# Optimization experiments

Hardware: AMD Instinct MI355X
Metric: run time of the kernel (lower is better)

Reference implementation:

```python
import itertools
import jax, jax.numpy as jnp
import numpy as np

B, S, D = 512, 49, 448
H, KD, RATIO, RES = 8, 32, 4, 7
EKD = KD * RATIO              # expanded key dim = 128
QKV_OUT = H * (2 * KD + EKD)  # 1536
MLP_HID = D * 4               # 1792
EPS = 1e-5
LS_INIT = 1e-5


def _build_bias_idxs():
    points = list(itertools.product(range(RES), range(RES)))
    offsets = {}
    idxs = []
    for p1 in points:
        for p2 in points:
            off = (abs(p1[0] - p2[0]), abs(p1[1] - p2[1]))
            if off not in offsets:
                offsets[off] = len(offsets)
            idxs.append(offsets[off])
    return np.asarray(idxs, dtype=np.int32).reshape(len(points), len(points)), len(offsets)


def setup_inputs() -> dict:
    key = jax.random.key(0)
    ks = jax.random.split(key, 10)
    idxs_np, n_off = _build_bias_idxs()  # (49,49), 49 unique offsets
    std = 0.02
    return {
        "hidden_states": jax.random.normal(ks[0], (B, S, D), jnp.float32),
        "ln1_g": jnp.ones((D,), jnp.float32),
        "ln1_b": jnp.zeros((D,), jnp.float32),
        "qkv_w": jax.random.normal(ks[1], (D, QKV_OUT), jnp.float32) * std,
        "qkv_b": jnp.zeros((QKV_OUT,), jnp.float32),
        "attention_biases": jax.random.normal(ks[2], (H, n_off), jnp.float32) * std,
        "proj_w": jax.random.normal(ks[3], (H * EKD, D), jnp.float32) * std,
        "proj_b": jnp.zeros((D,), jnp.float32),
        "ln2_g": jnp.ones((D,), jnp.float32),
        "ln2_b": jnp.zeros((D,), jnp.float32),
        "mlp_w1": jax.random.normal(ks[4], (D, MLP_HID), jnp.float32) * std,
        "mlp_b1": jnp.zeros((MLP_HID,), jnp.float32),
        "mlp_w2": jax.random.normal(ks[5], (MLP_HID, D), jnp.float32) * std,
        "mlp_b2": jnp.zeros((D,), jnp.float32),
        "ls1": jnp.full((D,), LS_INIT, jnp.float32),
        "ls2": jnp.full((D,), LS_INIT, jnp.float32),
        "attention_bias_idxs": jnp.asarray(idxs_np),
    }


def _layernorm(x, g, b):
    mu = jnp.mean(x, axis=-1, keepdims=True)
    var = jnp.mean(jnp.square(x - mu), axis=-1, keepdims=True)
    return (x - mu) * jax.lax.rsqrt(var + EPS) * g + b


def reference(hidden_states, ln1_g, ln1_b, qkv_w, qkv_b, attention_biases,
              proj_w, proj_b, ln2_g, ln2_b, mlp_w1, mlp_b1, mlp_w2, mlp_b2,
              ls1, ls2, attention_bias_idxs):
    x = hidden_states
    # --- token mixer (self-attention with relative-position bias) ---
    h = _layernorm(x, ln1_g, ln1_b)
    qkv = h @ qkv_w + qkv_b                           # [B,S,1536]
    qkv = qkv.reshape(B, S, H, 2 * KD + EKD)
    q, k, v = jnp.split(qkv, [KD, 2 * KD], axis=3)    # [B,S,H,32/32/128]
    scale = KD ** (-0.5)
    scores = jnp.einsum("bqhd,bkhd->bhqk", q, k) * scale
    bias = attention_biases[:, attention_bias_idxs]   # [H,S,S]
    probs = jax.nn.softmax(scores + bias[None], axis=-1)
    ctx = jnp.einsum("bhqk,bkhd->bqhd", probs, v).reshape(B, S, H * EKD)
    attn_out = ctx @ proj_w + proj_b                  # [B,S,D]
    # --- residual with layerscale (drop_path = identity in eval) ---
    x = x + ls1 * attn_out
    # --- MLP branch ---
    h2 = _layernorm(x, ln2_g, ln2_b)
    m = jax.nn.gelu(h2 @ mlp_w1 + mlp_b1, approximate=False)
    m = m @ mlp_w2 + mlp_b2
    x = x + ls2 * m
    return x
```

## Files before the change

kernel.cpp:

```cpp
#include <hip/hip_runtime.h>
#include <hip/hip_bf16.h>

#define BB 512
#define SS 49
#define DD 448
#define HH 8
#define QKVO 1536
#define MLPH 1792
#define MM (BB*SS)

using bf16_t = __hip_bfloat16;
typedef __attribute__((ext_vector_type(8))) short short8;
typedef __attribute__((ext_vector_type(4))) float f32x4;

__device__ __forceinline__ void gload_lds16(const void* g, void* l) {
  __builtin_amdgcn_global_load_lds(
      (const __attribute__((address_space(1))) void*)g,
      (__attribute__((address_space(3))) void*)l,
      16, 0, 0);
}

__global__ void prep_kernel(const float* __restrict__ qkv_w, const float* __restrict__ proj_w,
                            const float* __restrict__ w1, const float* __restrict__ w2,
                            const float* __restrict__ ab, const int* __restrict__ idxs,
                            bf16_t* __restrict__ qkv_wT, bf16_t* __restrict__ proj_wT,
                            bf16_t* __restrict__ w1T, bf16_t* __restrict__ w2T,
                            bf16_t* __restrict__ bias_pad)
{
  int idx = blockIdx.x * 256 + threadIdx.x;
  if (idx < 688128) {
    int n = idx / 448, k = idx % 448;
    qkv_wT[idx] = __float2bfloat16(qkv_w[k*1536 + n]);
  } else if ((idx -= 688128) < 458752) {
    int n = idx / 1024, k = idx % 1024;
    proj_wT[idx] = __float2bfloat16(proj_w[k*448 + n]);
  } else if ((idx -= 458752) < 802816) {
    int n = idx / 448, k = idx % 448;
    w1T[idx] = __float2bfloat16(w1[k*1792 + n]);
  } else if ((idx -= 802816) < 802816) {
    int n = idx / 1792, k = idx % 1792;
    w2T[idx] = __float2bfloat16(w2[k*448 + n]);
  } else if ((idx -= 802816) < 32768) {
    int h = idx >> 12, r = (idx >> 6) & 63, c = idx & 63;
    float v = (r < SS && c < SS) ? ab[h*49 + idxs[r*49 + c]] : -1e30f;
    bias_pad[idx] = __float2bfloat16(v);
  }
}

__global__ __launch_bounds__(256) void ln_kernel(const float* __restrict__ x,
                                                 const float* __restrict__ g,
                                                 const float* __restrict__ b,
                                                 bf16_t* __restrict__ out)
{
  const int w = threadIdx.x >> 6, lane = threadIdx.x & 63;
  const int row = blockIdx.x * 4 + w;
  const float* xr = x + (size_t)row * DD;
  float v[7];
  float s = 0.f;
#pragma unroll
  for (int j = 0; j < 7; ++j) { v[j] = xr[lane + 64*j]; s += v[j]; }
#pragma unroll
  for (int off = 32; off; off >>= 1) s += __shfl_xor(s, off, 64);
  const float mu = s * (1.0f/448.0f);
  float q = 0.f;
#pragma unroll
  for (int j = 0; j < 7; ++j) { float d = v[j] - mu; q += d*d; }
#pragma unroll
  for (int off = 32; off; off >>= 1) q += __shfl_xor(q, off, 64);
  const float rstd = rsqrtf(q * (1.0f/448.0f) + 1e-5f);
  bf16_t* orow = out + (size_t)row * DD;
#pragma unroll
  for (int j = 0; j < 7; ++j) {
    int c = lane + 64*j;
    orow[c] = __float2bfloat16((v[j] - mu) * rstd * g[c] + b[c]);
  }
}

__global__ __launch_bounds__(256) void red1_ln2_kernel(
    const float* __restrict__ x, const bf16_t* __restrict__ p0,
    const bf16_t* __restrict__ p1, const float* __restrict__ pb,
    const float* __restrict__ ls1, const float* __restrict__ g,
    const float* __restrict__ b, float* __restrict__ out, bf16_t* __restrict__ h2)
{
  const int w = threadIdx.x >> 6, lane = threadIdx.x & 63;
  const int row = blockIdx.x * 4 + w;
  const float* xr = x + (size_t)row * DD;
  const bf16_t* p0r = p0 + (size_t)row * DD;
  const bf16_t* p1r = p1 + (size_t)row * DD;
  float* orow = out + (size_t)row * DD;
  float v[7];
  float s = 0.f;
#pragma unroll
  for (int j = 0; j < 7; ++j) {
    const int c = lane + 64*j;
    const float pv = __bfloat162float(p0r[c]) + __bfloat162float(p1r[c]) + pb[c];
    v[j] = xr[c] + ls1[c] * pv;
    orow[c] = v[j];
    s += v[j];
  }
#pragma unroll
  for (int off = 32; off; off >>= 1) s += __shfl_xor(s, off, 64);
  const float mu = s * (1.0f/448.0f);
  float q = 0.f;
#pragma unroll
  for (int j = 0; j < 7; ++j) { float d = v[j] - mu; q += d*d; }
#pragma unroll
  for (int off = 32; off; off >>= 1) q += __shfl_xor(q, off, 64);
  const float rstd = rsqrtf(q * (1.0f/448.0f) + 1e-5f);
  bf16_t* hrow = h2 + (size_t)row * DD;
#pragma unroll
  for (int j = 0; j < 7; ++j) {
    const int c = lane + 64*j;
    hrow[c] = __float2bfloat16((v[j] - mu) * rstd * g[c] + b[c]);
  }
}

__global__ __launch_bounds__(256) void red2_kernel(
    const bf16_t* __restrict__ q0, const bf16_t* __restrict__ q1,
    const float* __restrict__ pb, const float* __restrict__ ls2,
    float* __restrict__ out)
{
  const int w = threadIdx.x >> 6, lane = threadIdx.x & 63;
  const int row = blockIdx.x * 4 + w;
  const bf16_t* q0r = q0 + (size_t)row * DD;
  const bf16_t* q1r = q1 + (size_t)row * DD;
  float* orow = out + (size_t)row * DD;
#pragma unroll
  for (int j = 0; j < 7; ++j) {
    const int c = lane + 64*j;
    const float pv = __bfloat162float(q0r[c]) + __bfloat162float(q1r[c]) + pb[c];
    orow[c] = orow[c] + ls2[c] * pv;
  }
}

enum { EP_BF16 = 0, EP_GELU = 2, EP_PART = 4 };

template<int EPI, int NSPLIT>
__global__ __launch_bounds__(256, 2) void gemmr_bf16(
    const bf16_t* __restrict__ A, const bf16_t* __restrict__ Bt,
    const float* __restrict__ bias, bf16_t* __restrict__ O0,
    bf16_t* __restrict__ O1, int N, int K, int gy)
{
  __shared__ __align__(16) char lds[32768];
  const int t = threadIdx.x;
  const int lane = t & 63;
  const int w = t >> 6;

  const int chunk = gridDim.x >> 3;
  const int swz = (blockIdx.x & 7) * chunk + (blockIdx.x >> 3);
  const int m0 = (swz / (gy * NSPLIT)) * 128;
  const int rr = swz % (gy * NSPLIT);
  const int n0 = (rr / NSPLIT) * 128;
  const int sp = rr % NSPLIT;
  const int ksub = K / NSPLIT;
  const int kbase = sp * ksub;

  const int fr = lane & 15;
  const int fq = lane >> 4;
  const int wm = (w >> 1) * 64;
  const int wn = (w & 1) * 64;

  f32x4 acc[4][4];
#pragma unroll
  for (int i = 0; i < 4; ++i)
#pragma unroll
    for (int j = 0; j < 4; ++j)
      acc[i][j] = f32x4{0.f, 0.f, 0.f, 0.f};

  const int rsub = t >> 3;
  const int g8 = (t & 7) ^ (rsub & 7);
  const int wbase = w * 1024;
  const int nkt = ksub >> 6;

  const bf16_t* gA[4];
  const bf16_t* gB[4];
#pragma unroll
  for (int i = 0; i < 4; ++i) {
    gA[i] = A + (size_t)(m0 + i*32 + rsub) * K + kbase + g8*8;
    int rb = n0 + i*32 + rsub;
    if (rb >= N) rb = N - 1;
    gB[i] = Bt + (size_t)rb * K + kbase + g8*8;
  }

  for (int kt = 0; kt < nkt; ++kt) {
    const int ko = kt << 6;
#pragma unroll
    for (int i = 0; i < 4; ++i) {
      gload_lds16(gA[i] + ko, lds + i*4096 + wbase);
      gload_lds16(gB[i] + ko, lds + 16384 + i*4096 + wbase);
    }
    __syncthreads();
#pragma unroll
    for (int kk = 0; kk < 2; ++kk) {
      short8 af[4], bfr[4];
#pragma unroll
      for (int i = 0; i < 4; ++i) {
        const int ra = wm + i*16 + fr;
        const int ca = (fq + kk*4) ^ (ra & 7);
        af[i] = *(const short8*)(lds + ra*128 + ca*16);
        const int rb2 = wn + i*16 + fr;
        const int cb = (fq + kk*4) ^ (rb2 & 7);
        bfr[i] = *(const short8*)(lds + 16384 + rb2*128 + cb*16);
      }
#pragma unroll
      for (int mi = 0; mi < 4; ++mi)
#pragma unroll
        for (int ni = 0; ni < 4; ++ni)
          acc[mi][ni] = __builtin_amdgcn_mfma_f32_16x16x32_bf16(af[mi], bfr[ni], acc[mi][ni], 0, 0, 0);
    }
    __syncthreads();
  }

  bf16_t* P = (NSPLIT == 2 && sp == 1) ? O1 : O0;
#pragma unroll
  for (int mi = 0; mi < 4; ++mi) {
#pragma unroll
    for (int ni = 0; ni < 4; ++ni) {
      const int col = n0 + wn + ni*16 + fr;
      if (col < N) {
        float bc = 0.f;
        if constexpr (EPI != EP_PART) bc = bias[col];
        const int row0 = m0 + wm + mi*16 + fq*4;
#pragma unroll
        for (int ri = 0; ri < 4; ++ri) {
          const size_t o = (size_t)(row0 + ri) * N + col;
          const float v = acc[mi][ni][ri] + bc;
          if constexpr (EPI == EP_GELU) {
            P[o] = __float2bfloat16(0.5f * v * (1.0f + erff(v * 0.7071067811865475f)));
          } else {
            P[o] = __float2bfloat16(v);
          }
        }
      }
    }
  }
}

__global__ __launch_bounds__(64) void attn_mfma_kernel(const bf16_t* __restrict__ qkv,
                                                       const bf16_t* __restrict__ bias_pad,
                                                       bf16_t* __restrict__ ctx)
{
  __shared__ __align__(16) bf16_t VsF[64*128];
  __shared__ __align__(16) bf16_t PsF[64*72];
  const int b = blockIdx.x >> 3, h = blockIdx.x & 7;
  const int l = threadIdx.x;
  const int fr = l & 15, g = l >> 4;
  const size_t base = ((size_t)b * SS) * QKVO + (size_t)h * 192;

  for (int c = l; c < 1024; c += 64) {
    const int j = c >> 4, ch = c & 15;
    const int jc = j < SS ? j : SS - 1;
    short8 v = *(const short8*)(qkv + base + (size_t)jc * QKVO + 64 + ch*8);
    *(short8*)(&VsF[j*128 + ((ch ^ (j >> 3)) & 15)*8]) = v;
  }

  short8 qf[4], kf[4];
#pragma unroll
  for (int mi = 0; mi < 4; ++mi) {
    int qr = mi*16 + fr; if (qr > SS-1) qr = SS-1;
    qf[mi] = *(const short8*)(qkv + base + (size_t)qr * QKVO + g*8);
    int kr = mi*16 + fr; if (kr > SS-1) kr = SS-1;
    kf[mi] = *(const short8*)(qkv + base + (size_t)kr * QKVO + 32 + g*8);
  }
  f32x4 sc[4][4];
#pragma unroll
  for (int mi = 0; mi < 4; ++mi)
#pragma unroll
    for (int ni = 0; ni < 4; ++ni)
      sc[mi][ni] = f32x4{0.f,0.f,0.f,0.f};
#pragma unroll
  for (int mi = 0; mi < 4; ++mi)
#pragma unroll
    for (int ni = 0; ni < 4; ++ni)
      sc[mi][ni] = __builtin_amdgcn_mfma_f32_16x16x32_bf16(qf[mi], kf[ni], sc[mi][ni], 0, 0, 0);

  const float scale = 0.17677669529663687f;
  const bf16_t* bp = bias_pad + (size_t)h * 4096;
#pragma unroll
  for (int mi = 0; mi < 4; ++mi) {
#pragma unroll
    for (int ri = 0; ri < 4; ++ri) {
      const int r = mi*16 + g*4 + ri;
      float v0 = sc[mi][0][ri]*scale + __bfloat162float(bp[r*64 +      fr]);
      float v1 = sc[mi][1][ri]*scale + __bfloat162float(bp[r*64 + 16 + fr]);
      float v2 = sc[mi][2][ri]*scale + __bfloat162float(bp[r*64 + 32 + fr]);
      float v3 = sc[mi][3][ri]*scale + __bfloat162float(bp[r*64 + 48 + fr]);
      float m = fmaxf(fmaxf(v0, v1), fmaxf(v2, v3));
#pragma unroll
      for (int off = 8; off; off >>= 1) m = fmaxf(m, __shfl_xor(m, off, 64));
      v0 = __expf(v0 - m); v1 = __expf(v1 - m);
      v2 = __expf(v2 - m); v3 = __expf(v3 - m);
      float s = v0 + v1 + v2 + v3;
#pragma unroll
      for (int off = 8; off; off >>= 1) s += __shfl_xor(s, off, 64);
      const float inv = 1.0f / s;
      PsF[r*72 +      fr] = __float2bfloat16(v0 * inv);
      PsF[r*72 + 16 + fr] = __float2bfloat16(v1 * inv);
      PsF[r*72 + 32 + fr] = __float2bfloat16(v2 * inv);
      PsF[r*72 + 48 + fr] = __float2bfloat16(v3 * inv);
    }
  }
  __syncthreads();

  short8 pf[4][2];
#pragma unroll
  for (int mi = 0; mi < 4; ++mi)
#pragma unroll
    for (int ks = 0; ks < 2; ++ks)
      pf[mi][ks] = *(const short8*)(&PsF[(mi*16 + fr)*72 + ks*32 + g*8]);

#pragma unroll
  for (int ni = 0; ni < 8; ++ni) {
    const int e = ni*16 + fr;
    short8 vf[2];
#pragma unroll
    for (int ks = 0; ks < 2; ++ks) {
      const int jb = ks*32 + g*8;
#pragma unroll
      for (int jj = 0; jj < 8; ++jj) {
        const int j = jb + jj;
        const int ch = ((e >> 3) ^ (j >> 3)) & 15;
        vf[ks][jj] = *(const short*)(&VsF[j*128 + ch*8 + (e & 7)]);
      }
    }
    f32x4 acc2[4];
#pragma unroll
    for (int mi = 0; mi < 4; ++mi) acc2[mi] = f32x4{0.f,0.f,0.f,0.f};
#pragma unroll
    for (int ks = 0; ks < 2; ++ks)
#pragma unroll
      for (int mi = 0; mi < 4; ++mi)
        acc2[mi] = __builtin_amdgcn_mfma_f32_16x16x32_bf16(pf[mi][ks], vf[ks], acc2[mi], 0, 0, 0);
#pragma unroll
    for (int mi = 0; mi < 4; ++mi) {
#pragma unroll
      for (int ri = 0; ri < 4; ++ri) {
        const int q = mi*16 + g*4 + ri;
        if (q < SS)
          ctx[((size_t)b * SS + q) * 1024 + h*128 + e] = __float2bfloat16(acc2[mi][ri]);
      }
    }
  }
}

extern "C" void kernel_launch(void* const* d_in, const int* in_sizes, int n_in,
                              void* d_out, int out_size, void* d_ws, size_t ws_size,
                              hipStream_t stream) {
  const float* x      = (const float*)d_in[0];
  const float* ln1_g  = (const float*)d_in[1];
  const float* ln1_b  = (const float*)d_in[2];
  const float* qkv_w  = (const float*)d_in[3];
  const float* qkv_b  = (const float*)d_in[4];
  const float* ab     = (const float*)d_in[5];
  const float* proj_w = (const float*)d_in[6];
  const float* proj_b = (const float*)d_in[7];
  const float* ln2_g  = (const float*)d_in[8];
  const float* ln2_b  = (const float*)d_in[9];
  const float* w1     = (const float*)d_in[10];
  const float* b1     = (const float*)d_in[11];
  const float* w2     = (const float*)d_in[12];
  const float* b2     = (const float*)d_in[13];
  const float* ls1    = (const float*)d_in[14];
  const float* ls2    = (const float*)d_in[15];
  const int*   idxs   = (const int*)d_in[16];
  float* out = (float*)d_out;
  char* ws = (char*)d_ws;

  bf16_t* h_buf    = (bf16_t*)(ws);
  bf16_t* qkv_buf  = (bf16_t*)(ws + 22478848);
  bf16_t* ctx_buf  = (bf16_t*)(ws + 99549184);
  bf16_t* m_buf    = (bf16_t*)(ws + 22478848);
  bf16_t* p0       = (bf16_t*)(ws + 22478848);
  bf16_t* p1       = (bf16_t*)(ws + 44957696);
  bf16_t* q0       = (bf16_t*)(ws);
  bf16_t* q1       = (bf16_t*)(ws + 112394240);
  bf16_t* qkv_wT   = (bf16_t*)(ws + 150929408);
  bf16_t* proj_wT  = (bf16_t*)(ws + 152305664);
  bf16_t* w1T      = (bf16_t*)(ws + 153223168);
  bf16_t* w2T      = (bf16_t*)(ws + 154828800);
  bf16_t* bias_pad = (bf16_t*)(ws + 156434432);

  const int prep_total = 688128 + 458752 + 802816 + 802816 + 32768;
  prep_kernel<<<(prep_total + 255)/256, 256, 0, stream>>>(
      qkv_w, proj_w, w1, w2, ab, idxs, qkv_wT, proj_wT, w1T, w2T, bias_pad);

  ln_kernel<<<MM/4, 256, 0, stream>>>(x, ln1_g, ln1_b, h_buf);

  gemmr_bf16<EP_BF16, 1><<<196*12, 256, 0, stream>>>(
      h_buf, qkv_wT, qkv_b, qkv_buf, nullptr, QKVO, DD, 12);

  attn_mfma_kernel<<<BB*HH, 64, 0, stream>>>(qkv_buf, bias_pad, ctx_buf);

  gemmr_bf16<EP_PART, 2><<<196*4*2, 256, 0, stream>>>(
      ctx_buf, proj_wT, nullptr, p0, p1, DD, 1024, 4);

  red1_ln2_kernel<<<MM/4, 256, 0, stream>>>(
      x, p0, p1, proj_b, ls1, ln2_g, ln2_b, out, h_buf);

  gemmr_bf16<EP_GELU, 1><<<196*14, 256, 0, stream>>>(
      h_buf, w1T, b1, m_buf, nullptr, MLPH, DD, 14);

  gemmr_bf16<EP_PART, 2><<<196*4*2, 256, 0, stream>>>(
      m_buf, w2T, nullptr, q0, q1, DD, MLPH, 4);

  red2_kernel<<<MM/4, 256, 0, stream>>>(q0, q1, b2, ls2, out);
}
```

Before: 324.8 us.

## Add 256x128-tile bf16 GEMM with XCD-aware block remap for QKV and MLP1

Adds a new 512-thread bf16 MFMA GEMM with 256x128 output tiles, a K-step of 64 staged through swizzled LDS via direct global-to-LDS loads, and a block remap that gives each XCD a contiguous range of tiles. The bias and GELU epilogue is written through LDS so rows are stored with wide 16-byte writes. It replaces the 128x128 kernel for the QKV projection and the first MLP GEMM, aiming for more operand reuse per tile and better L2 locality. The LDS tile is single-buffered and uses about 68 KB, which limits occupancy below the declared launch bound. Load latency may therefore not be hidden well across the seven K iterations.

```diff
diff --git a/kernel.cpp b/kernel.cpp
--- a/kernel.cpp
+++ b/kernel.cpp
@@ -134,6 +134,116 @@
 }
 
 enum { EP_BF16 = 0, EP_GELU = 2, EP_PART = 4 };
+
+template<int EPI>
+__global__ __launch_bounds__(512, 4) void gemm256_bf16(
+    const bf16_t* __restrict__ A, const bf16_t* __restrict__ Bt,
+    const float* __restrict__ bias, bf16_t* __restrict__ O,
+    int N, int K, int gy)
+{
+  __shared__ __align__(16) char lds[69632];
+  const int t = threadIdx.x;
+  const int lane = t & 63;
+  const int w = t >> 6;
+
+  const int nwg = gridDim.x;
+  const int q8 = nwg >> 3, r8 = nwg & 7;
+  const int xcd = blockIdx.x & 7, bix = blockIdx.x >> 3;
+  const int wg = (xcd < r8 ? xcd*(q8+1) : r8*(q8+1) + (xcd-r8)*q8) + bix;
+  const int m0 = (wg / gy) * 256;
+  const int n0 = (wg % gy) * 128;
+
+  const int fr = lane & 15;
+  const int fq = lane >> 4;
+  const int wm = (w >> 1) * 64;
+  const int wn = (w & 1) * 64;
+
+  f32x4 acc[4][4];
+#pragma unroll
+  for (int i = 0; i < 4; ++i)
+#pragma unroll
+    for (int j = 0; j < 4; ++j)
+      acc[i][j] = f32x4{0.f, 0.f, 0.f, 0.f};
+
+  const int rsub = t >> 3;
+  const int g8 = (t & 7) ^ (rsub & 7);
+  const int wbase = w * 1024;
+  const int nkt = K >> 6;
+
+  const bf16_t* gA[4];
+  const bf16_t* gB[2];
+#pragma unroll
+  for (int i = 0; i < 4; ++i)
+    gA[i] = A + (size_t)(m0 + i*64 + rsub) * K + g8*8;
+#pragma unroll
+  for (int i = 0; i < 2; ++i) {
+    int rb = n0 + i*64 + rsub;
+    if (rb >= N) rb = N - 1;
+    gB[i] = Bt + (size_t)rb * K + g8*8;
+  }
+
+  for (int kt = 0; kt < nkt; ++kt) {
+    const int ko = kt << 6;
+#pragma unroll
+    for (int i = 0; i < 4; ++i)
+      gload_lds16(gA[i] + ko, lds + i*8192 + wbase);
+#pragma unroll
+    for (int i = 0; i < 2; ++i)
+      gload_lds16(gB[i] + ko, lds + 32768 + i*8192 + wbase);
+    __syncthreads();
+#pragma unroll
+    for (int kk = 0; kk < 2; ++kk) {
+      short8 af[4], bfr[4];
+#pragma unroll
+      for (int i = 0; i < 4; ++i) {
+        const int ra = wm + i*16 + fr;
+        const int ca = (fq + kk*4) ^ (ra & 7);
+        af[i] = *(const short8*)(lds + ra*128 + ca*16);
+        const int rb2 = wn + i*16 + fr;
+        const int cb = (fq + kk*4) ^ (rb2 & 7);
+        bfr[i] = *(const short8*)(lds + 32768 + rb2*128 + cb*16);
+      }
+#pragma unroll
+      for (int mi = 0; mi < 4; ++mi)
+#pragma unroll
+        for (int ni = 0; ni < 4; ++ni)
+          acc[mi][ni] = __builtin_amdgcn_mfma_f32_16x16x32_bf16(af[mi], bfr[ni], acc[mi][ni], 0, 0, 0);
+    }
+    __syncthreads();
+  }
+
+  bf16_t* lbf = (bf16_t*)lds;
+#pragma unroll
+  for (int mi = 0; mi < 4; ++mi) {
+#pragma unroll
+    for (int ni = 0; ni < 4; ++ni) {
+      const int col = wn + ni*16 + fr;
+      const float bc = bias[n0 + col];
+      const int row0 = wm + mi*16 + fq*4;
+#pragma unroll
+      for (int ri = 0; ri < 4; ++ri) {
+        float v = acc[mi][ni][ri] + bc;
+        if constexpr (EPI == EP_GELU)
+          v = 0.5f * v * (1.0f + erff(v * 0.7071067811865475f));
+        lbf[(row0 + ri)*136 + col] = __float2bfloat16(v);
+      }
+    }
+  }
+  __syncthreads();
+
+  const int rl = t >> 3;
+  const int ll = t & 7;
+#pragma unroll
+  for (int j = 0; j < 4; ++j) {
+    const int r = rl + j*64;
+    const bf16_t* src = &lbf[r*136 + ll*16];
+    short8 v0 = *(const short8*)(src);
+    short8 v1 = *(const short8*)(src + 8);
+    bf16_t* dst = O + (size_t)(m0 + r) * N + n0 + ll*16;
+    *(short8*)(dst) = v0;
+    *(short8*)(dst + 8) = v1;
+  }
+}
 
 template<int EPI, int NSPLIT>
 __global__ __launch_bounds__(256, 2) void gemmr_bf16(
@@ -386,8 +496,8 @@
 
   ln_kernel<<<MM/4, 256, 0, stream>>>(x, ln1_g, ln1_b, h_buf);
 
-  gemmr_bf16<EP_BF16, 1><<<196*12, 256, 0, stream>>>(
-      h_buf, qkv_wT, qkv_b, qkv_buf, nullptr, QKVO, DD, 12);
+  gemm256_bf16<EP_BF16><<<98*12, 512, 0, stream>>>(
+      h_buf, qkv_wT, qkv_b, qkv_buf, QKVO, DD, 12);
 
   attn_mfma_kernel<<<BB*HH, 64, 0, stream>>>(qkv_buf, bias_pad, ctx_buf);
 
@@ -397,8 +507,8 @@
   red1_ln2_kernel<<<MM/4, 256, 0, stream>>>(
       x, p0, p1, proj_b, ls1, ln2_g, ln2_b, out, h_buf);
 
-  gemmr_bf16<EP_GELU, 1><<<196*14, 256, 0, stream>>>(
-      h_buf, w1T, b1, m_buf, nullptr, MLPH, DD, 14);
+  gemm256_bf16<EP_GELU><<<98*14, 512, 0, stream>>>(
+      h_buf, w1T, b1, m_buf, MLPH, DD, 14);
 
   gemmr_bf16<EP_PART, 2><<<196*4*2, 256, 0, stream>>>(
       m_buf, w2T, nullptr, q0, q1, DD, MLPH, 4);
```

Measured after the change: 334.0 us. +2.8%, slower.
